# Performance work log

Measured on AMD Instinct MI355X. Metric: run time of the kernel, lower is better.

The kernel has to match this reference:

```python
import jax, jax.numpy as jnp
import numpy as np

E, D, H = 1024, 64, 16   # embed_dim, head_dim, num_heads
B, L = 8, 4096


def _ln(x, g, b, eps=1e-5):
    m = jnp.mean(x, axis=-1, keepdims=True)
    v = jnp.var(x, axis=-1, keepdims=True)
    return (x - m) / jnp.sqrt(v + eps) * g + b


def setup_inputs() -> dict:
    key = jax.random.key(0)
    ks = jax.random.split(key, 10)
    s_e = 1.0 / np.sqrt(E)
    s_d = 1.0 / np.sqrt(D)
    f32 = jnp.float32
    return {
        "emb": jax.random.normal(ks[0], (B, L, E), f32),
        # per-head linears stacked on a leading head axis
        "Wa": jax.random.normal(ks[1], (H, E, D), f32) * s_e,
        "ba": jnp.zeros((H, D), f32),
        "Wb": jax.random.normal(ks[2], (H, E, D), f32) * s_e,
        "bb": jnp.zeros((H, D), f32),
        "Wc": jax.random.normal(ks[3], (H, D, D), f32) * s_d,
        "bc": jnp.zeros((H, D), f32),
        "head_w": jnp.ones((H,), f32),
        "hn_g": jnp.ones((H, D), f32),
        "hn_b": jnp.zeros((H, D), f32),
        "Wd": jax.random.normal(ks[4], (E, D), f32) * s_e,
        "bd": jnp.zeros((D,), f32),
        "W1": jax.random.normal(ks[5], (D, 4 * D), f32) * s_d,
        "b1": jnp.zeros((4 * D,), f32),
        "W2": jax.random.normal(ks[6], (4 * D, D), f32) * (1.0 / np.sqrt(4 * D)),
        "b2": jnp.zeros((D,), f32),
        "Wp": jax.random.normal(ks[7], (D, D), f32) * s_d,
        "bp": jnp.zeros((D,), f32),
        "ng": jnp.ones((D,), f32),
        "nb": jnp.zeros((D,), f32),
    }


def reference(emb, Wa, ba, Wb, bb, Wc, bc, head_w, hn_g, hn_b,
              Wd, bd, W1, b1, W2, b2, Wp, bp, ng, nb):
    b_sz, seq_len, _ = emb.shape
    n_heads, d_head = ba.shape

    # gates depend only on x_t -> precompute for all t, all heads  [B,L,H,D]
    a = jnp.tanh(jnp.einsum('ble,hed->blhd', emb, Wa) + ba)
    bt = jnp.einsum('ble,hed->blhd', emb, Wb) + bb

    # linear recurrence h_t = a_t * h_{t-1} + b_t over time
    a_t = jnp.moveaxis(a, 1, 0)    # [L,B,H,D]
    b_t = jnp.moveaxis(bt, 1, 0)

    def step(h, ab):
        at, btt = ab
        h = at * h + btt
        return h, h

    h0 = jnp.zeros((b_sz, n_heads, d_head), emb.dtype)
    _, hs = jax.lax.scan(step, h0, (a_t, b_t))
    hs = jnp.moveaxis(hs, 0, 1)    # [B,L,H,D]

    dx = emb @ Wd + bd             # [B,L,D] shared D(x_t)

    out = jnp.einsum('blhd,hde->blhe', hs, Wc) + bc + dx[:, :, None, :]
    out = _ln(out, hn_g, hn_b)     # per-head LayerNorm, gamma/beta [H,D]

    sum_heads = dx + jnp.einsum('h,blhd->bld', head_w, out)
    z = sum_heads / n_heads

    u = z + _ln(z, ng, nb)
    ffn = jax.nn.gelu(u @ W1 + b1, approximate=False) @ W2 + b2
    h_out = u + ffn
    return h_out @ Wp + bp
```

## Files before the change

### kernel.cpp

```cpp
#include <hip/hip_runtime.h>
#include <hip/hip_bf16.h>
#include <math.h>
#include <stdint.h>

#define E_DIM 1024
#define D_DIM 64
#define H_DIM 16
#define B_SZ  8
#define L_SEQ 4096
#define M_TOK (B_SZ * L_SEQ)
#define NCAT  2112
#define NPAD  2176
#define CHUNK 128
#define NCHUNK (L_SEQ / CHUNK)

typedef float  f32x4  __attribute__((ext_vector_type(4)));
typedef __bf16 bf16x8 __attribute__((ext_vector_type(8)));
typedef __bf16 bf16x4 __attribute__((ext_vector_type(4)));

__device__ __forceinline__ float tanh_fast(float v) {
  float vc = fminf(fmaxf(v, -12.f), 12.f);
  float ex = __expf(vc + vc);
  return (ex - 1.f) / (ex + 1.f);
}
__device__ __forceinline__ void load_lds16(const void* g, void* l) {
  __builtin_amdgcn_global_load_lds(
      (const __attribute__((address_space(1))) void*)g,
      (__attribute__((address_space(3))) void*)l, 16, 0, 0);
}

__global__ __launch_bounds__(256) void cast_emb(const float* __restrict__ in,
                                                bf16x4* __restrict__ out) {
  int i = blockIdx.x * 256 + threadIdx.x;
  float4 v = ((const float4*)in)[i];
  bf16x4 o;
  o[0] = (__bf16)v.x; o[1] = (__bf16)v.y; o[2] = (__bf16)v.z; o[3] = (__bf16)v.w;
  out[i] = o;
}

__global__ __launch_bounds__(256) void pack_w(
    const float* __restrict__ Wa, const float* __restrict__ ba,
    const float* __restrict__ Wb, const float* __restrict__ bb,
    const float* __restrict__ Wd, const float* __restrict__ bd,
    __bf16* __restrict__ wcat, float* __restrict__ bias) {
  int gid = blockIdx.x * 256 + threadIdx.x;
  int n = gid >> 10, k = gid & 1023;
  float w, bv;
  if (n < 1024) {
    int h = n >> 6, d = n & 63;
    w = Wa[((h << 10) | k) * 64 + d]; bv = ba[n];
  } else if (n < 2048) {
    int nn = n - 1024; int h = nn >> 6, d = nn & 63;
    w = Wb[((h << 10) | k) * 64 + d]; bv = bb[nn];
  } else if (n < NCAT) {
    int d = n - 2048;
    w = Wd[k * 64 + d];  bv = bd[d];
  } else { w = 0.f; bv = 0.f; }
  wcat[n * 1024 + k] = (__bf16)w;
  if (k == 0) bias[n] = bv;
}

__global__ __launch_bounds__(256) void pack_ffnw(
    const float* __restrict__ W1, const float* __restrict__ W2,
    const float* __restrict__ Wp,
    __bf16* __restrict__ g_w1t, __bf16* __restrict__ g_w2t,
    __bf16* __restrict__ g_wpt) {
  int idx = blockIdx.x * 256 + threadIdx.x;
  if (idx < 16384) {
    int k = idx >> 8, n = idx & 255;
    g_w1t[n * 72 + k] = (__bf16)W1[idx];
  } else if (idx < 32768) {
    int j = idx - 16384; int k = j >> 6, n = j & 63;
    g_w2t[n * 256 + (((k >> 3) ^ (n & 7)) << 3) + (k & 7)] = (__bf16)W2[j];
  } else {
    int j = idx - 32768; int k = j >> 6, n = j & 63;
    g_wpt[n * 72 + k] = (__bf16)Wp[j];
  }
}

__global__ __launch_bounds__(256) void pack_wct(const float* __restrict__ Wc,
                                                __bf16* __restrict__ wct) {
  int idx = blockIdx.x * 256 + threadIdx.x;
  int h = idx >> 12, e = (idx >> 6) & 63, d = idx & 63;
  wct[idx] = (__bf16)Wc[h * 4096 + d * 64 + e];
}

__global__ __launch_bounds__(256) void gemm_fused(
    const __bf16* __restrict__ A, const __bf16* __restrict__ Wt,
    const float* __restrict__ bias,
    __bf16* __restrict__ abuf, __bf16* __restrict__ bbuf, float* __restrict__ dxbuf) {
  __shared__ __bf16 As[128 * 64];
  __shared__ __bf16 Bs[128 * 64];
  const int nt = blockIdx.x, mt = blockIdx.y;
  const int m0 = mt * 128, n0 = nt * 128;
  const int t = threadIdx.x, w = t >> 6, l = t & 63;
  const int lr = l >> 3, lc = l & 7;
  const int swz = lc ^ lr;
  const int q = l >> 4, c16 = l & 15;

  f32x4 acc[4][4];
#pragma unroll
  for (int i = 0; i < 4; ++i)
#pragma unroll
    for (int j = 0; j < 4; ++j) acc[i][j] = (f32x4)(0.f);

  const __bf16* gA = A  + (size_t)(m0 + w * 8 + lr) * 1024 + swz * 8;
  const __bf16* gB = Wt + (size_t)(n0 + w * 8 + lr) * 1024 + swz * 8;
  __bf16* lA = As + w * 512;
  __bf16* lB = Bs + w * 512;

  for (int kk = 0; kk < 16; ++kk) {
    const int k0 = kk * 64;
#pragma unroll
    for (int r = 0; r < 4; ++r) {
      load_lds16(gA + (size_t)r * 32 * 1024 + k0, lA + r * 2048);
      load_lds16(gB + (size_t)r * 32 * 1024 + k0, lB + r * 2048);
    }
    __syncthreads();
#pragma unroll
    for (int ks = 0; ks < 2; ++ks) {
      bf16x8 af[4], bfr[4];
#pragma unroll
      for (int i = 0; i < 4; ++i) {
        int mloc = (w >> 1) * 64 + i * 16 + c16;
        int cp = (ks * 4 + q) ^ (mloc & 7);
        af[i] = *(const bf16x8*)(As + mloc * 64 + cp * 8);
      }
#pragma unroll
      for (int j = 0; j < 4; ++j) {
        int nloc = (w & 1) * 64 + j * 16 + c16;
        int cp = (ks * 4 + q) ^ (nloc & 7);
        bfr[j] = *(const bf16x8*)(Bs + nloc * 64 + cp * 8);
      }
#pragma unroll
      for (int i = 0; i < 4; ++i)
#pragma unroll
        for (int j = 0; j < 4; ++j)
          acc[i][j] = __builtin_amdgcn_mfma_f32_16x16x32_bf16(af[i], bfr[j], acc[i][j], 0, 0, 0);
    }
    __syncthreads();
  }

#pragma unroll
  for (int j = 0; j < 4; ++j) {
    int n = n0 + (w & 1) * 64 + j * 16 + c16;
    float bv = bias[n];
#pragma unroll
    for (int i = 0; i < 4; ++i) {
      int mbase = m0 + (w >> 1) * 64 + i * 16 + q * 4;
#pragma unroll
      for (int r = 0; r < 4; ++r) {
        float v = acc[i][j][r] + bv;
        int m = mbase + r;
        if (n < 1024)            abuf[(size_t)m * 1024 + n] = (__bf16)tanh_fast(v);
        else if (n < 2048)       bbuf[(size_t)m * 1024 + (n - 1024)] = (__bf16)v;
        else if (n < NCAT)       dxbuf[m * 64 + (n - 2048)] = v;
      }
    }
  }
}

__global__ __launch_bounds__(256) void scan_local_bf(
    __bf16* __restrict__ abuf, __bf16* __restrict__ bbuf,
    float* __restrict__ cA, float* __restrict__ cH) {
  int bc = blockIdx.x;
  int n4 = threadIdx.x * 4;
  size_t base = (size_t)bc * CHUNK * 1024 + n4;
  float p[4] = {1.f, 1.f, 1.f, 1.f}, h[4] = {0.f, 0.f, 0.f, 0.f};
  for (int s = 0; s < CHUNK; ++s) {
    size_t idx = base + (size_t)s * 1024;
    bf16x4 av = *(const bf16x4*)(abuf + idx);
    bf16x4 bv = *(const bf16x4*)(bbuf + idx);
    bf16x4 po, ho;
#pragma unroll
    for (int i = 0; i < 4; ++i) {
      float a = (float)av[i];
      p[i] *= a;
      h[i] = fmaf(a, h[i], (float)bv[i]);
      po[i] = (__bf16)p[i];
      ho[i] = (__bf16)h[i];
    }
    *(bf16x4*)(abuf + idx) = po;
    *(bf16x4*)(bbuf + idx) = ho;
  }
  int ci = bc * 1024 + n4;
  float4 pv = {p[0], p[1], p[2], p[3]};
  float4 hv = {h[0], h[1], h[2], h[3]};
  *(float4*)(cA + ci) = pv;
  *(float4*)(cH + ci) = hv;
}

__global__ __launch_bounds__(256) void scan_carry(
    const float* __restrict__ cA, const float* __restrict__ cH, float* __restrict__ cIn) {
  int gid = blockIdx.x * 256 + threadIdx.x;
  int n = gid & 1023, b = gid >> 10;
  float carry = 0.f;
  for (int c = 0; c < NCHUNK; ++c) {
    int idx = (b * NCHUNK + c) * 1024 + n;
    cIn[idx] = carry;
    carry = fmaf(cA[idx], carry, cH[idx]);
  }
}

__global__ __launch_bounds__(256) void heads_mfma(
    const __bf16* __restrict__ ahat, const __bf16* __restrict__ hloc,
    const float* __restrict__ dxbuf, const float* __restrict__ cIn,
    const __bf16* __restrict__ wct, const float* __restrict__ bch,
    const float* __restrict__ head_w, const float* __restrict__ hng,
    const float* __restrict__ hnb, const float* __restrict__ ng,
    const float* __restrict__ nbv, float* __restrict__ ubuf) {
  __shared__ float carryS[1024];
  const int tid = threadIdx.x, w = tid >> 6, l = tid & 63;
  const int q = l >> 4, c16 = l & 15;
  const int m0 = blockIdx.x * 64;
  const int b = m0 >> 12, c = (m0 & 4095) >> 7;
  const int cb = (b * NCHUNK + c) * 1024;
  ((float4*)carryS)[tid] = ((const float4*)(cIn + cb))[tid];
  __syncthreads();

  const size_t arow = (size_t)(m0 + w * 16 + c16) * 1024;

  float dxr[4][4];
#pragma unroll
  for (int j = 0; j < 4; ++j)
#pragma unroll
    for (int r = 0; r < 4; ++r)
      dxr[j][r] = dxbuf[(m0 + w * 16 + q * 4 + r) * 64 + j * 16 + c16];

  f32x4 accum[4];
#pragma unroll
  for (int j = 0; j < 4; ++j) accum[j] = (f32x4)(0.f);

  for (int h = 0; h < H_DIM; ++h) {
    bf16x8 af[2];
#pragma unroll
    for (int ks = 0; ks < 2; ++ks) {
      int dbase = h * 64 + ks * 32 + q * 8;
      bf16x8 av = *(const bf16x8*)(ahat + arow + dbase);
      bf16x8 hv = *(const bf16x8*)(hloc + arow + dbase);
      float4 cv0 = *(const float4*)(carryS + dbase);
      float4 cv1 = *(const float4*)(carryS + dbase + 4);
      bf16x8 hf;
      hf[0] = (__bf16)fmaf((float)av[0], cv0.x, (float)hv[0]);
      hf[1] = (__bf16)fmaf((float)av[1], cv0.y, (float)hv[1]);
      hf[2] = (__bf16)fmaf((float)av[2], cv0.z, (float)hv[2]);
      hf[3] = (__bf16)fmaf((float)av[3], cv0.w, (float)hv[3]);
      hf[4] = (__bf16)fmaf((float)av[4], cv1.x, (float)hv[4]);
      hf[5] = (__bf16)fmaf((float)av[5], cv1.y, (float)hv[5]);
      hf[6] = (__bf16)fmaf((float)av[6], cv1.z, (float)hv[6]);
      hf[7] = (__bf16)fmaf((float)av[7], cv1.w, (float)hv[7]);
      af[ks] = hf;
    }
    f32x4 acc[4];
#pragma unroll
    for (int j = 0; j < 4; ++j) acc[j] = (f32x4)(0.f);
#pragma unroll
    for (int ks = 0; ks < 2; ++ks)
#pragma unroll
      for (int j = 0; j < 4; ++j) {
        bf16x8 bf = *(const bf16x8*)(wct + h * 4096 + (j * 16 + c16) * 64 + ks * 32 + q * 8);
        acc[j] = __builtin_amdgcn_mfma_f32_16x16x32_bf16(af[ks], bf, acc[j], 0, 0, 0);
      }
    float hw = head_w[h];
    float g4[4], be4[4], bb4[4];
#pragma unroll
    for (int j = 0; j < 4; ++j) {
      int nh = h * 64 + j * 16 + c16;
      g4[j] = hng[nh]; bb4[j] = hnb[nh]; be4[j] = bch[nh];
    }
#pragma unroll
    for (int r = 0; r < 4; ++r) {
      float v0 = acc[0][r] + be4[0] + dxr[0][r];
      float v1 = acc[1][r] + be4[1] + dxr[1][r];
      float v2 = acc[2][r] + be4[2] + dxr[2][r];
      float v3 = acc[3][r] + be4[3] + dxr[3][r];
      float s  = (v0 + v1) + (v2 + v3);
      float s2 = fmaf(v0, v0, fmaf(v1, v1, fmaf(v2, v2, v3 * v3)));
#pragma unroll
      for (int off = 1; off < 16; off <<= 1) {
        s  += __shfl_xor(s, off, 64);
        s2 += __shfl_xor(s2, off, 64);
      }
      float mean = s * (1.f / 64.f);
      float var  = fmaf(s2, 1.f / 64.f, -mean * mean);
      float inv  = rsqrtf(fmaxf(var, 0.f) + 1e-5f);
      accum[0][r] = fmaf(hw, fmaf((v0 - mean) * inv, g4[0], bb4[0]), accum[0][r]);
      accum[1][r] = fmaf(hw, fmaf((v1 - mean) * inv, g4[1], bb4[1]), accum[1][r]);
      accum[2][r] = fmaf(hw, fmaf((v2 - mean) * inv, g4[2], bb4[2]), accum[2][r]);
      accum[3][r] = fmaf(hw, fmaf((v3 - mean) * inv, g4[3], bb4[3]), accum[3][r]);
    }
  }
  float ng4[4], nb4[4];
#pragma unroll
  for (int j = 0; j < 4; ++j) { ng4[j] = ng[j * 16 + c16]; nb4[j] = nbv[j * 16 + c16]; }
#pragma unroll
  for (int r = 0; r < 4; ++r) {
    float z0 = (dxr[0][r] + accum[0][r]) * (1.f / 16.f);
    float z1 = (dxr[1][r] + accum[1][r]) * (1.f / 16.f);
    float z2 = (dxr[2][r] + accum[2][r]) * (1.f / 16.f);
    float z3 = (dxr[3][r] + accum[3][r]) * (1.f / 16.f);
    float s  = (z0 + z1) + (z2 + z3);
    float s2 = fmaf(z0, z0, fmaf(z1, z1, fmaf(z2, z2, z3 * z3)));
#pragma unroll
    for (int off = 1; off < 16; off <<= 1) {
      s  += __shfl_xor(s, off, 64);
      s2 += __shfl_xor(s2, off, 64);
    }
    float mean = s * (1.f / 64.f);
    float var  = fmaf(s2, 1.f / 64.f, -mean * mean);
    float inv  = rsqrtf(fmaxf(var, 0.f) + 1e-5f);
    int mrow = (m0 + w * 16 + q * 4 + r) * 64;
    ubuf[mrow + 0 * 16 + c16] = z0 + fmaf((z0 - mean) * inv, ng4[0], nb4[0]);
    ubuf[mrow + 1 * 16 + c16] = z1 + fmaf((z1 - mean) * inv, ng4[1], nb4[1]);
    ubuf[mrow + 2 * 16 + c16] = z2 + fmaf((z2 - mean) * inv, ng4[2], nb4[2]);
    ubuf[mrow + 3 * 16 + c16] = z3 + fmaf((z3 - mean) * inv, ng4[3], nb4[3]);
  }
}

__global__ __launch_bounds__(256) void ffn_mfma(
    const float* __restrict__ ubuf,
    const __bf16* __restrict__ g_w1t, const __bf16* __restrict__ g_w2t,
    const __bf16* __restrict__ g_wpt,
    const float* __restrict__ b1, const float* __restrict__ b2,
    const float* __restrict__ bp, float* __restrict__ out) {
  __shared__ __bf16 pool[32768];
  const int tid = threadIdx.x, w = tid >> 6, l = tid & 63;
  const int q = l >> 4, c16 = l & 15;
  const int m0 = blockIdx.x * 64;
  __bf16* Us  = pool;
  __bf16* W1T = pool + 4608;
  __bf16* T1S = pool;
  __bf16* W2T = pool + 16384;
  __bf16* HoS = pool;
  __bf16* WpT = pool + 4608;

#pragma unroll
  for (int r = 0; r < 16; ++r) {
    int idx = r * 256 + tid, m = idx >> 6, e = idx & 63;
    Us[m * 72 + e] = (__bf16)ubuf[(size_t)(m0 + m) * 64 + e];
  }
#pragma unroll
  for (int r = 0; r < 9; ++r)
    load_lds16(g_w1t + (size_t)(r * 256 + tid) * 8,
               (char*)pool + 9216 + (r * 256 + w * 64) * 16);
  __syncthreads();

  f32x4 acc1[16];
#pragma unroll
  for (int j = 0; j < 16; ++j) acc1[j] = (f32x4)(0.f);
#pragma unroll
  for (int ks = 0; ks < 2; ++ks) {
    bf16x8 a = *(const bf16x8*)(Us + (w * 16 + c16) * 72 + ks * 32 + q * 8);
#pragma unroll
    for (int j = 0; j < 16; ++j) {
      bf16x8 b = *(const bf16x8*)(W1T + (j * 16 + c16) * 72 + ks * 32 + q * 8);
      acc1[j] = __builtin_amdgcn_mfma_f32_16x16x32_bf16(a, b, acc1[j], 0, 0, 0);
    }
  }
  __syncthreads();

#pragma unroll
  for (int r = 0; r < 8; ++r)
    load_lds16(g_w2t + (size_t)(r * 256 + tid) * 8,
               (char*)pool + 32768 + (r * 256 + w * 64) * 16);
#pragma unroll
  for (int j = 0; j < 16; ++j) {
    int n = j * 16 + c16;
    float bv = b1[n];
#pragma unroll
    for (int rr = 0; rr < 4; ++rr) {
      int m = w * 16 + q * 4 + rr;
      float x = acc1[j][rr] + bv;
      float g = 0.5f * x * (1.f + erff(x * 0.70710678118654752f));
      T1S[m * 256 + (((n >> 3) ^ (m & 7)) << 3) + (n & 7)] = (__bf16)g;
    }
  }
  __syncthreads();

  f32x4 acc2[4];
#pragma unroll
  for (int j = 0; j < 4; ++j) acc2[j] = (f32x4)(0.f);
  const int arow2 = w * 16 + c16;
#pragma unroll
  for (int ks = 0; ks < 8; ++ks) {
    bf16x8 a = *(const bf16x8*)(T1S + arow2 * 256 + (((ks * 4 + q) ^ (arow2 & 7)) << 3));
#pragma unroll
    for (int j = 0; j < 4; ++j) {
      int brow = j * 16 + c16;
      bf16x8 b = *(const bf16x8*)(W2T + brow * 256 + (((ks * 4 + q) ^ (brow & 7)) << 3));
      acc2[j] = __builtin_amdgcn_mfma_f32_16x16x32_bf16(a, b, acc2[j], 0, 0, 0);
    }
  }
  __syncthreads();

#pragma unroll
  for (int r = 0; r < 2; ++r)
    load_lds16(g_wpt + (size_t)(r * 256 + tid) * 8,
               (char*)pool + 9216 + (r * 256 + w * 64) * 16);
  if (tid < 64)
    load_lds16(g_wpt + (size_t)(512 + tid) * 8, (char*)pool + 9216 + 512 * 16);
#pragma unroll
  for (int j = 0; j < 4; ++j) {
    int e = j * 16 + c16;
    float bv = b2[e];
#pragma unroll
    for (int rr = 0; rr < 4; ++rr) {
      int m = w * 16 + q * 4 + rr;
      float hres = acc2[j][rr] + bv + ubuf[(size_t)(m0 + m) * 64 + e];
      HoS[m * 72 + e] = (__bf16)hres;
    }
  }
  __syncthreads();

  f32x4 acc3[4];
#pragma unroll
  for (int j = 0; j < 4; ++j) acc3[j] = (f32x4)(0.f);
#pragma unroll
  for (int ks = 0; ks < 2; ++ks) {
    bf16x8 a = *(const bf16x8*)(HoS + (w * 16 + c16) * 72 + ks * 32 + q * 8);
#pragma unroll
    for (int j = 0; j < 4; ++j) {
      bf16x8 b = *(const bf16x8*)(WpT + (j * 16 + c16) * 72 + ks * 32 + q * 8);
      acc3[j] = __builtin_amdgcn_mfma_f32_16x16x32_bf16(a, b, acc3[j], 0, 0, 0);
    }
  }
#pragma unroll
  for (int j = 0; j < 4; ++j) {
    int e = j * 16 + c16;
    float bv = bp[e];
#pragma unroll
    for (int rr = 0; rr < 4; ++rr) {
      int m = w * 16 + q * 4 + rr;
      out[(size_t)(m0 + m) * 64 + e] = acc3[j][rr] + bv;
    }
  }
}

extern "C" void kernel_launch(void* const* d_in, const int* in_sizes, int n_in,
                              void* d_out, int out_size, void* d_ws, size_t ws_size,
                              hipStream_t stream) {
  const float* emb    = (const float*)d_in[0];
  const float* Wa     = (const float*)d_in[1];
  const float* ba     = (const float*)d_in[2];
  const float* Wb     = (const float*)d_in[3];
  const float* bb     = (const float*)d_in[4];
  const float* Wc     = (const float*)d_in[5];
  const float* bc     = (const float*)d_in[6];
  const float* head_w = (const float*)d_in[7];
  const float* hn_g   = (const float*)d_in[8];
  const float* hn_b   = (const float*)d_in[9];
  const float* Wd     = (const float*)d_in[10];
  const float* bd     = (const float*)d_in[11];
  const float* W1     = (const float*)d_in[12];
  const float* b1     = (const float*)d_in[13];
  const float* W2     = (const float*)d_in[14];
  const float* b2     = (const float*)d_in[15];
  const float* Wp     = (const float*)d_in[16];
  const float* bp     = (const float*)d_in[17];
  const float* ng     = (const float*)d_in[18];
  const float* nb     = (const float*)d_in[19];
  float* out = (float*)d_out;

  char* wsp = (char*)d_ws;
  size_t off = 0;
  auto alloc = [&](size_t bytes) -> char* {
    char* p = wsp + off;
    off += (bytes + 255) & ~(size_t)255;
    return p;
  };
  __bf16* embh  = (__bf16*)alloc((size_t)M_TOK * E_DIM * 2);
  __bf16* wcat  = (__bf16*)alloc((size_t)NPAD * E_DIM * 2);
  float*  bias  = (float*)alloc((size_t)NPAD * 4);
  __bf16* abuf  = (__bf16*)alloc((size_t)M_TOK * 1024 * 2);
  __bf16* bbuf  = (__bf16*)alloc((size_t)M_TOK * 1024 * 2);
  float*  dxbuf = (float*)alloc((size_t)M_TOK * 64 * 4);
  float*  cA    = (float*)alloc((size_t)256 * 1024 * 4);
  float*  cH    = (float*)alloc((size_t)256 * 1024 * 4);
  float*  cIn   = (float*)alloc((size_t)256 * 1024 * 4);
  float*  ubuf  = (float*)alloc((size_t)M_TOK * 64 * 4);
  __bf16* g_w1t = (__bf16*)alloc((size_t)256 * 72 * 2);
  __bf16* g_w2t = (__bf16*)alloc((size_t)64 * 256 * 2);
  __bf16* g_wpt = (__bf16*)alloc((size_t)64 * 72 * 2);
  __bf16* wct   = (__bf16*)alloc((size_t)H_DIM * 64 * 64 * 2);

  cast_emb<<<dim3(32768), dim3(256), 0, stream>>>(emb, (bf16x4*)embh);
  pack_w<<<dim3(8704), dim3(256), 0, stream>>>(Wa, ba, Wb, bb, Wd, bd, wcat, bias);
  pack_ffnw<<<dim3(144), dim3(256), 0, stream>>>(W1, W2, Wp, g_w1t, g_w2t, g_wpt);
  pack_wct<<<dim3(256), dim3(256), 0, stream>>>(Wc, wct);
  gemm_fused<<<dim3(17, 256), dim3(256), 0, stream>>>(embh, wcat, bias, abuf, bbuf, dxbuf);
  scan_local_bf<<<dim3(256), dim3(256), 0, stream>>>(abuf, bbuf, cA, cH);
  scan_carry<<<dim3(32), dim3(256), 0, stream>>>(cA, cH, cIn);
  heads_mfma<<<dim3(512), dim3(256), 0, stream>>>(abuf, bbuf, dxbuf, cIn, wct, bc,
                                                  head_w, hn_g, hn_b, ng, nb, ubuf);
  ffn_mfma<<<dim3(512), dim3(256), 0, stream>>>(ubuf, g_w1t, g_w2t, g_wpt,
                                                b1, b2, bp, out);
}
```

Measured before the change: 596.3 us.

## Merge prep kernels, remap GEMM grid per XCD, make FFN wave-local

Four small packing and cast kernels become one prep launch, which removes launch gaps. The GEMM grid is flattened and remapped so that each XCD works on a contiguous band of M tiles, which should improve L2 reuse of A rows. The FFN kernel becomes wave-independent: weights are read straight from global memory or cache instead of being staged through LDS with block barriers, and only per-wave scratch in LDS is used with wave barriers. The cost is more global loads of the weights per wave, though the weights are small and should stay cached.

```diff
diff --git a/kernel.cpp b/kernel.cpp
--- a/kernel.cpp
+++ b/kernel.cpp
@@ -29,60 +29,57 @@
       (__attribute__((address_space(3))) void*)l, 16, 0, 0);
 }
 
-__global__ __launch_bounds__(256) void cast_emb(const float* __restrict__ in,
-                                                bf16x4* __restrict__ out) {
-  int i = blockIdx.x * 256 + threadIdx.x;
-  float4 v = ((const float4*)in)[i];
-  bf16x4 o;
-  o[0] = (__bf16)v.x; o[1] = (__bf16)v.y; o[2] = (__bf16)v.z; o[3] = (__bf16)v.w;
-  out[i] = o;
-}
-
-__global__ __launch_bounds__(256) void pack_w(
+__global__ __launch_bounds__(256) void prep(
+    const float* __restrict__ emb, bf16x4* __restrict__ embh,
     const float* __restrict__ Wa, const float* __restrict__ ba,
     const float* __restrict__ Wb, const float* __restrict__ bb,
     const float* __restrict__ Wd, const float* __restrict__ bd,
-    __bf16* __restrict__ wcat, float* __restrict__ bias) {
-  int gid = blockIdx.x * 256 + threadIdx.x;
-  int n = gid >> 10, k = gid & 1023;
-  float w, bv;
-  if (n < 1024) {
-    int h = n >> 6, d = n & 63;
-    w = Wa[((h << 10) | k) * 64 + d]; bv = ba[n];
-  } else if (n < 2048) {
-    int nn = n - 1024; int h = nn >> 6, d = nn & 63;
-    w = Wb[((h << 10) | k) * 64 + d]; bv = bb[nn];
-  } else if (n < NCAT) {
-    int d = n - 2048;
-    w = Wd[k * 64 + d];  bv = bd[d];
-  } else { w = 0.f; bv = 0.f; }
-  wcat[n * 1024 + k] = (__bf16)w;
-  if (k == 0) bias[n] = bv;
-}
-
-__global__ __launch_bounds__(256) void pack_ffnw(
+    __bf16* __restrict__ wcat, float* __restrict__ bias,
     const float* __restrict__ W1, const float* __restrict__ W2,
     const float* __restrict__ Wp,
     __bf16* __restrict__ g_w1t, __bf16* __restrict__ g_w2t,
-    __bf16* __restrict__ g_wpt) {
-  int idx = blockIdx.x * 256 + threadIdx.x;
-  if (idx < 16384) {
-    int k = idx >> 8, n = idx & 255;
-    g_w1t[n * 72 + k] = (__bf16)W1[idx];
-  } else if (idx < 32768) {
-    int j = idx - 16384; int k = j >> 6, n = j & 63;
-    g_w2t[n * 256 + (((k >> 3) ^ (n & 7)) << 3) + (k & 7)] = (__bf16)W2[j];
+    __bf16* __restrict__ g_wpt,
+    const float* __restrict__ Wc, __bf16* __restrict__ wct) {
+  const int blk = blockIdx.x, tid = threadIdx.x;
+  if (blk < 32768) {
+    int i = blk * 256 + tid;
+    float4 v = ((const float4*)emb)[i];
+    bf16x4 o;
+    o[0] = (__bf16)v.x; o[1] = (__bf16)v.y; o[2] = (__bf16)v.z; o[3] = (__bf16)v.w;
+    embh[i] = o;
+  } else if (blk < 41472) {
+    int gid = (blk - 32768) * 256 + tid;
+    int n = gid >> 10, k = gid & 1023;
+    float w, bv;
+    if (n < 1024) {
+      int h = n >> 6, d = n & 63;
+      w = Wa[((h << 10) | k) * 64 + d]; bv = ba[n];
+    } else if (n < 2048) {
+      int nn = n - 1024; int h = nn >> 6, d = nn & 63;
+      w = Wb[((h << 10) | k) * 64 + d]; bv = bb[nn];
+    } else if (n < NCAT) {
+      int d = n - 2048;
+      w = Wd[k * 64 + d];  bv = bd[d];
+    } else { w = 0.f; bv = 0.f; }
+    wcat[n * 1024 + k] = (__bf16)w;
+    if (k == 0) bias[n] = bv;
+  } else if (blk < 41616) {
+    int idx = (blk - 41472) * 256 + tid;
+    if (idx < 16384) {
+      int k = idx >> 8, n = idx & 255;
+      g_w1t[n * 72 + k] = (__bf16)W1[idx];
+    } else if (idx < 32768) {
+      int j = idx - 16384; int k = j >> 6, n = j & 63;
+      g_w2t[n * 256 + k] = (__bf16)W2[j];
+    } else {
+      int j = idx - 32768; int k = j >> 6, n = j & 63;
+      g_wpt[n * 72 + k] = (__bf16)Wp[j];
+    }
   } else {
-    int j = idx - 32768; int k = j >> 6, n = j & 63;
-    g_wpt[n * 72 + k] = (__bf16)Wp[j];
-  }
-}
-
-__global__ __launch_bounds__(256) void pack_wct(const float* __restrict__ Wc,
-                                                __bf16* __restrict__ wct) {
-  int idx = blockIdx.x * 256 + threadIdx.x;
-  int h = idx >> 12, e = (idx >> 6) & 63, d = idx & 63;
-  wct[idx] = (__bf16)Wc[h * 4096 + d * 64 + e];
+    int idx = (blk - 41616) * 256 + tid;
+    int h = idx >> 12, e = (idx >> 6) & 63, d = idx & 63;
+    wct[idx] = (__bf16)Wc[h * 4096 + d * 64 + e];
+  }
 }
 
 __global__ __launch_bounds__(256) void gemm_fused(
@@ -91,7 +88,10 @@
     __bf16* __restrict__ abuf, __bf16* __restrict__ bbuf, float* __restrict__ dxbuf) {
   __shared__ __bf16 As[128 * 64];
   __shared__ __bf16 Bs[128 * 64];
-  const int nt = blockIdx.x, mt = blockIdx.y;
+  const int bb = blockIdx.x;
+  const int xcd = bb & 7, wv = bb >> 3;
+  const int nt = wv % 17;
+  const int mt = xcd * 32 + wv / 17;
   const int m0 = mt * 128, n0 = nt * 128;
   const int t = threadIdx.x, w = t >> 6, l = t & 63;
   const int lr = l >> 3, lc = l & 7;
@@ -317,110 +317,92 @@
   }
 }
 
-__global__ __launch_bounds__(256) void ffn_mfma(
+__global__ __launch_bounds__(256) void ffn_wave(
     const float* __restrict__ ubuf,
     const __bf16* __restrict__ g_w1t, const __bf16* __restrict__ g_w2t,
     const __bf16* __restrict__ g_wpt,
     const float* __restrict__ b1, const float* __restrict__ b2,
     const float* __restrict__ bp, float* __restrict__ out) {
-  __shared__ __bf16 pool[32768];
+  __shared__ __bf16 tls[4][4096];
   const int tid = threadIdx.x, w = tid >> 6, l = tid & 63;
   const int q = l >> 4, c16 = l & 15;
-  const int m0 = blockIdx.x * 64;
-  __bf16* Us  = pool;
-  __bf16* W1T = pool + 4608;
-  __bf16* T1S = pool;
-  __bf16* W2T = pool + 16384;
-  __bf16* HoS = pool;
-  __bf16* WpT = pool + 4608;
-
-#pragma unroll
-  for (int r = 0; r < 16; ++r) {
-    int idx = r * 256 + tid, m = idx >> 6, e = idx & 63;
-    Us[m * 72 + e] = (__bf16)ubuf[(size_t)(m0 + m) * 64 + e];
-  }
-#pragma unroll
-  for (int r = 0; r < 9; ++r)
-    load_lds16(g_w1t + (size_t)(r * 256 + tid) * 8,
-               (char*)pool + 9216 + (r * 256 + w * 64) * 16);
-  __syncthreads();
+  const int m0w = blockIdx.x * 64 + w * 16;
+  __bf16* T = tls[w];
+
+  bf16x8 ua[2];
+#pragma unroll
+  for (int ks = 0; ks < 2; ++ks) {
+    const float* up = ubuf + (size_t)(m0w + c16) * 64 + ks * 32 + q * 8;
+    float4 v0 = *(const float4*)up;
+    float4 v1 = *(const float4*)(up + 4);
+    bf16x8 tt;
+    tt[0] = (__bf16)v0.x; tt[1] = (__bf16)v0.y; tt[2] = (__bf16)v0.z; tt[3] = (__bf16)v0.w;
+    tt[4] = (__bf16)v1.x; tt[5] = (__bf16)v1.y; tt[6] = (__bf16)v1.z; tt[7] = (__bf16)v1.w;
+    ua[ks] = tt;
+  }
 
   f32x4 acc1[16];
 #pragma unroll
   for (int j = 0; j < 16; ++j) acc1[j] = (f32x4)(0.f);
 #pragma unroll
-  for (int ks = 0; ks < 2; ++ks) {
-    bf16x8 a = *(const bf16x8*)(Us + (w * 16 + c16) * 72 + ks * 32 + q * 8);
-#pragma unroll
-    for (int j = 0; j < 16; ++j) {
-      bf16x8 b = *(const bf16x8*)(W1T + (j * 16 + c16) * 72 + ks * 32 + q * 8);
-      acc1[j] = __builtin_amdgcn_mfma_f32_16x16x32_bf16(a, b, acc1[j], 0, 0, 0);
-    }
-  }
-  __syncthreads();
-
-#pragma unroll
-  for (int r = 0; r < 8; ++r)
-    load_lds16(g_w2t + (size_t)(r * 256 + tid) * 8,
-               (char*)pool + 32768 + (r * 256 + w * 64) * 16);
+  for (int j = 0; j < 16; ++j) {
+    const __bf16* bp1 = g_w1t + (j * 16 + c16) * 72 + q * 8;
+    bf16x8 b0 = *(const bf16x8*)bp1;
+    bf16x8 b1f = *(const bf16x8*)(bp1 + 32);
+    acc1[j] = __builtin_amdgcn_mfma_f32_16x16x32_bf16(ua[0], b0, acc1[j], 0, 0, 0);
+    acc1[j] = __builtin_amdgcn_mfma_f32_16x16x32_bf16(ua[1], b1f, acc1[j], 0, 0, 0);
+  }
+
 #pragma unroll
   for (int j = 0; j < 16; ++j) {
     int n = j * 16 + c16;
     float bv = b1[n];
 #pragma unroll
     for (int rr = 0; rr < 4; ++rr) {
-      int m = w * 16 + q * 4 + rr;
+      int tok = q * 4 + rr;
       float x = acc1[j][rr] + bv;
       float g = 0.5f * x * (1.f + erff(x * 0.70710678118654752f));
-      T1S[m * 256 + (((n >> 3) ^ (m & 7)) << 3) + (n & 7)] = (__bf16)g;
-    }
-  }
-  __syncthreads();
+      T[tok * 256 + (((n >> 3) ^ (tok & 7)) << 3) + (n & 7)] = (__bf16)g;
+    }
+  }
+  __builtin_amdgcn_wave_barrier();
 
   f32x4 acc2[4];
 #pragma unroll
   for (int j = 0; j < 4; ++j) acc2[j] = (f32x4)(0.f);
-  const int arow2 = w * 16 + c16;
 #pragma unroll
   for (int ks = 0; ks < 8; ++ks) {
-    bf16x8 a = *(const bf16x8*)(T1S + arow2 * 256 + (((ks * 4 + q) ^ (arow2 & 7)) << 3));
+    bf16x8 a = *(const bf16x8*)(T + c16 * 256 + (((ks * 4 + q) ^ (c16 & 7)) << 3));
 #pragma unroll
     for (int j = 0; j < 4; ++j) {
-      int brow = j * 16 + c16;
-      bf16x8 b = *(const bf16x8*)(W2T + brow * 256 + (((ks * 4 + q) ^ (brow & 7)) << 3));
+      bf16x8 b = *(const bf16x8*)(g_w2t + (j * 16 + c16) * 256 + ks * 32 + q * 8);
       acc2[j] = __builtin_amdgcn_mfma_f32_16x16x32_bf16(a, b, acc2[j], 0, 0, 0);
     }
   }
-  __syncthreads();
-
-#pragma unroll
-  for (int r = 0; r < 2; ++r)
-    load_lds16(g_wpt + (size_t)(r * 256 + tid) * 8,
-               (char*)pool + 9216 + (r * 256 + w * 64) * 16);
-  if (tid < 64)
-    load_lds16(g_wpt + (size_t)(512 + tid) * 8, (char*)pool + 9216 + 512 * 16);
+  __builtin_amdgcn_wave_barrier();
+
 #pragma unroll
   for (int j = 0; j < 4; ++j) {
     int e = j * 16 + c16;
     float bv = b2[e];
 #pragma unroll
     for (int rr = 0; rr < 4; ++rr) {
-      int m = w * 16 + q * 4 + rr;
-      float hres = acc2[j][rr] + bv + ubuf[(size_t)(m0 + m) * 64 + e];
-      HoS[m * 72 + e] = (__bf16)hres;
-    }
-  }
-  __syncthreads();
+      int tok = q * 4 + rr;
+      float hres = acc2[j][rr] + bv + ubuf[(size_t)(m0w + tok) * 64 + e];
+      T[tok * 64 + (((e >> 3) ^ (tok & 7)) << 3) + (e & 7)] = (__bf16)hres;
+    }
+  }
+  __builtin_amdgcn_wave_barrier();
 
   f32x4 acc3[4];
 #pragma unroll
   for (int j = 0; j < 4; ++j) acc3[j] = (f32x4)(0.f);
 #pragma unroll
   for (int ks = 0; ks < 2; ++ks) {
-    bf16x8 a = *(const bf16x8*)(HoS + (w * 16 + c16) * 72 + ks * 32 + q * 8);
+    bf16x8 a = *(const bf16x8*)(T + c16 * 64 + (((ks * 4 + q) ^ (c16 & 7)) << 3));
 #pragma unroll
     for (int j = 0; j < 4; ++j) {
-      bf16x8 b = *(const bf16x8*)(WpT + (j * 16 + c16) * 72 + ks * 32 + q * 8);
+      bf16x8 b = *(const bf16x8*)(g_wpt + (j * 16 + c16) * 72 + ks * 32 + q * 8);
       acc3[j] = __builtin_amdgcn_mfma_f32_16x16x32_bf16(a, b, acc3[j], 0, 0, 0);
     }
   }
@@ -429,10 +411,8 @@
     int e = j * 16 + c16;
     float bv = bp[e];
 #pragma unroll
-    for (int rr = 0; rr < 4; ++rr) {
-      int m = w * 16 + q * 4 + rr;
-      out[(size_t)(m0 + m) * 64 + e] = acc3[j][rr] + bv;
-    }
+    for (int rr = 0; rr < 4; ++rr)
+      out[(size_t)(m0w + q * 4 + rr) * 64 + e] = acc3[j][rr] + bv;
   }
 }
 
@@ -483,15 +463,14 @@
   __bf16* g_wpt = (__bf16*)alloc((size_t)64 * 72 * 2);
   __bf16* wct   = (__bf16*)alloc((size_t)H_DIM * 64 * 64 * 2);
 
-  cast_emb<<<dim3(32768), dim3(256), 0, stream>>>(emb, (bf16x4*)embh);
-  pack_w<<<dim3(8704), dim3(256), 0, stream>>>(Wa, ba, Wb, bb, Wd, bd, wcat, bias);
-  pack_ffnw<<<dim3(144), dim3(256), 0, stream>>>(W1, W2, Wp, g_w1t, g_w2t, g_wpt);
-  pack_wct<<<dim3(256), dim3(256), 0, stream>>>(Wc, wct);
-  gemm_fused<<<dim3(17, 256), dim3(256), 0, stream>>>(embh, wcat, bias, abuf, bbuf, dxbuf);
+  prep<<<dim3(41872), dim3(256), 0, stream>>>(
+      emb, (bf16x4*)embh, Wa, ba, Wb, bb, Wd, bd, wcat, bias,
+      W1, W2, Wp, g_w1t, g_w2t, g_wpt, Wc, wct);
+  gemm_fused<<<dim3(4352), dim3(256), 0, stream>>>(embh, wcat, bias, abuf, bbuf, dxbuf);
   scan_local_bf<<<dim3(256), dim3(256), 0, stream>>>(abuf, bbuf, cA, cH);
   scan_carry<<<dim3(32), dim3(256), 0, stream>>>(cA, cH, cIn);
   heads_mfma<<<dim3(512), dim3(256), 0, stream>>>(abuf, bbuf, dxbuf, cIn, wct, bc,
                                                   head_w, hn_g, hn_b, ng, nb, ubuf);
-  ffn_mfma<<<dim3(512), dim3(256), 0, stream>>>(ubuf, g_w1t, g_w2t, g_wpt,
+  ffn_wave<<<dim3(512), dim3(256), 0, stream>>>(ubuf, g_w1t, g_w2t, g_wpt,
                                                 b1, b2, bp, out);
 }
```

Result: slower. 610.9 us (+2.5%).
